# Optimization experiments

Hardware: AMD Instinct MI355X
Metric: run time of the kernel (lower is better)

Reference implementation:

```python
import jax, jax.numpy as jnp
import numpy as np
from jax import lax

NPOINTS = 1024
K = 32
EPS = 1e-5


def fps(xyz, npoints):
    # Furthest point sampling. xyz: (B, N, 3) -> idx (B, npoints) int32.
    B, N, _ = xyz.shape
    def step(carry, _):
        dists, last = carry
        last_xyz = jnp.take_along_axis(xyz, last[:, None, None], axis=1)  # (B,1,3)
        d = jnp.sum((xyz - last_xyz) ** 2, axis=-1)  # (B,N)
        dists = jnp.minimum(dists, d)
        nxt = jnp.argmax(dists, axis=-1).astype(jnp.int32)
        return (dists, nxt), last
    init = (jnp.full((B, N), 1e10, xyz.dtype), jnp.zeros((B,), jnp.int32))
    _, idx = lax.scan(step, init, None, length=npoints)
    return idx.T  # (B, npoints)


def knn_idx(new_xyz, xyz, k):
    # new_xyz (B,S,3), xyz (B,N,3) -> (B,S,k) indices of k nearest neighbors.
    d = (jnp.sum(new_xyz ** 2, -1)[:, :, None]
         - 2.0 * jnp.einsum('bsc,bnc->bsn', new_xyz, xyz)
         + jnp.sum(xyz ** 2, -1)[:, None, :])  # (B,S,N)
    _, idx = lax.top_k(-d, k)
    return idx


def batch_gather(x, idx):
    # x (B, N, C), idx (B, ...) -> (B, ..., C)
    return jax.vmap(lambda a, i: a[i])(x, idx)


def bn(x, g, b, axes):
    # training-mode batchnorm over `axes`, channel on last axis
    m = jnp.mean(x, axes, keepdims=True)
    v = jnp.var(x, axes, keepdims=True)
    return g * (x - m) * lax.rsqrt(v + EPS) + b


def setup_inputs() -> dict:
    key = jax.random.key(0)
    ks = jax.random.split(key, 8)
    B, N, D, Cw, OUT = 16, 4096, 64, 64, 64
    inp = {
        'xyz': jax.random.uniform(ks[0], (B, N, 3), jnp.float32),
        'feature': jax.random.normal(ks[1], (B, D, N), jnp.float32),
        'w0': jax.random.normal(ks[2], (3, Cw), jnp.float32) * 0.3,
        'b0': jnp.zeros((Cw,), jnp.float32),
        'g0': jnp.ones((Cw,), jnp.float32),
        'be0': jnp.zeros((Cw,), jnp.float32),
        'w1': jax.random.normal(ks[3], (Cw, Cw), jnp.float32) * 0.1,
        'b1': jnp.zeros((Cw,), jnp.float32),
        'g1': jnp.ones((Cw,), jnp.float32),
        'be1': jnp.zeros((Cw,), jnp.float32),
        'w2': jax.random.normal(ks[4], (Cw, Cw), jnp.float32) * 0.1,
        'b2': jnp.zeros((Cw,), jnp.float32),
        'g2': jnp.ones((Cw,), jnp.float32),
        'be2': jnp.zeros((Cw,), jnp.float32),
        'wf': jax.random.normal(ks[5], (D * Cw, OUT), jnp.float32) * 0.02,
        'bf': jnp.zeros((OUT,), jnp.float32),
        'gf': jnp.ones((OUT,), jnp.float32),
        'bef': jnp.zeros((OUT,), jnp.float32),
    }
    return inp


def reference(xyz, feature, w0, b0, g0, be0, w1, b1, g1, be1, w2, b2, g2, be2, wf, bf, gf, bef):
    B, N, _ = xyz.shape
    # FPS + gather centroids
    fps_idx = fps(xyz, NPOINTS)                    # (B, S)
    new_xyz = batch_gather(xyz, fps_idx)           # (B, S, 3)
    # kNN grouping
    idx = knn_idx(new_xyz, xyz, K)                 # (B, S, K)
    grouped_xyz = batch_gather(xyz, idx) - new_xyz[:, :, None, :]   # (B,S,K,3)
    feat_nlast = jnp.swapaxes(feature, 1, 2)       # (B, N, D)
    grouped_feature = batch_gather(feat_nlast, idx)  # (B, S, K, D)
    # WeightNet: 1x1 conv MLP 3 -> Cw -> Cw -> Cw with BN+ReLU
    h = grouped_xyz
    for w, b, g, be in ((w0, b0, g0, be0), (w1, b1, g1, be1), (w2, b2, g2, be2)):
        h = jax.nn.relu(bn(h @ w + b, g, be, (0, 1, 2)))  # (B,S,K,Cw)
    weights = h
    # per-centroid matmul: (B,S,D,K) x (B,S,K,Cw) -> (B,S,D,Cw)
    nf = jnp.einsum('bskd,bskw->bsdw', grouped_feature, weights)
    nf = nf.reshape(B, NPOINTS, -1)                # (B, S, D*Cw)
    # final Conv1d(1x1) + BN1d + ReLU
    out = jax.nn.relu(bn(nf @ wf + bf, gf, bef, (0, 1)))  # (B, S, OUT)
    out = jnp.swapaxes(out, 1, 2)                  # (B, OUT, S)
    return (new_xyz, out)
```

## Files before the change

### kernel.cpp

```cpp
#include <hip/hip_runtime.h>

#define NBATCH 16
#define NPTS   4096
#define NSAMP  1024
#define NKNN   32
#define NROWS  (NBATCH*NSAMP*NKNN)
#define BN_EPS 1e-5f
#define H1PAD  66
#define KNN_CAP 512

typedef __attribute__((ext_vector_type(4))) float f32x4;
typedef __attribute__((ext_vector_type(8))) short bf16x8;
union frag_u { unsigned u[4]; bf16x8 h; uint4 u4; };

__device__ __forceinline__ unsigned pack_bf16pair(float a, float b) {
    unsigned ua = __float_as_uint(a); ua += 0x7FFFu + ((ua >> 16) & 1u);
    unsigned ub = __float_as_uint(b); ub += 0x7FFFu + ((ub >> 16) & 1u);
    return (ua >> 16) | (ub & 0xFFFF0000u);
}

__global__ __launch_bounds__(256) void fps_kernel(const float* __restrict__ xyz,
                                                  float* __restrict__ newxyz)
{
    const int b = blockIdx.x;
    const int tid = threadIdx.x;
    const int wv = tid >> 6;
    const float* xb = xyz + (size_t)b * NPTS * 3;
    __shared__ float xs[NPTS];
    __shared__ float ys[NPTS];
    __shared__ float zs[NPTS];
    __shared__ __align__(16) float4 red[2][4];
    __shared__ __align__(16) float nxs[NSAMP*3];
    float px[16], py[16], pz[16], dmin[16];
    {
        float arr[48];
        const float4* s4 = (const float4*)(xb + (size_t)tid * 48);
        #pragma unroll
        for (int i = 0; i < 12; ++i) *(float4*)&arr[i*4] = s4[i];
        #pragma unroll
        for (int j = 0; j < 16; ++j) {
            px[j] = arr[3*j]; py[j] = arr[3*j+1]; pz[j] = arr[3*j+2];
            const int p = tid * 16 + j;
            xs[p] = px[j]; ys[p] = py[j]; zs[p] = pz[j];
            dmin[j] = 1e10f;
        }
    }
    if (tid == 0) { nxs[0] = xb[0]; nxs[1] = xb[1]; nxs[2] = xb[2]; }
    __syncthreads();
    float lx = xs[0], ly = ys[0], lz = zs[0];
    for (int t = 1; t < NSAMP; ++t) {
        float bv = -1.0f;
        #pragma unroll
        for (int j = 0; j < 16; ++j) {
            const float dx = __fsub_rn(px[j], lx);
            const float dy = __fsub_rn(py[j], ly);
            const float dz = __fsub_rn(pz[j], lz);
            const float d = __fadd_rn(__fadd_rn(__fmul_rn(dx,dx), __fmul_rn(dy,dy)), __fmul_rn(dz,dz));
            const float nd = fminf(dmin[j], d);
            dmin[j] = nd;
            bv = fmaxf(bv, nd);
        }
        int lj = 0;
        #pragma unroll
        for (int j = 15; j >= 0; --j) if (dmin[j] == bv) lj = j;
        const int bi_lane = tid * 16 + lj;
        float mv = bv;
        {
            int s_;
            s_ = __builtin_amdgcn_mov_dpp(__float_as_int(mv), 0x111, 0xf, 0xf, true);
            mv = fmaxf(mv, __int_as_float(s_));
            s_ = __builtin_amdgcn_mov_dpp(__float_as_int(mv), 0x112, 0xf, 0xf, true);
            mv = fmaxf(mv, __int_as_float(s_));
            s_ = __builtin_amdgcn_mov_dpp(__float_as_int(mv), 0x114, 0xf, 0xf, true);
            mv = fmaxf(mv, __int_as_float(s_));
            s_ = __builtin_amdgcn_mov_dpp(__float_as_int(mv), 0x118, 0xf, 0xf, true);
            mv = fmaxf(mv, __int_as_float(s_));
            s_ = __builtin_amdgcn_mov_dpp(__float_as_int(mv), 0x142, 0xf, 0xf, true);
            mv = fmaxf(mv, __int_as_float(s_));
            s_ = __builtin_amdgcn_mov_dpp(__float_as_int(mv), 0x143, 0xf, 0xf, true);
            mv = fmaxf(mv, __int_as_float(s_));
        }
        mv = __int_as_float(__builtin_amdgcn_readlane(__float_as_int(mv), 63));
        const unsigned long long mask = __ballot(bv == mv);
        const int winner = __ffsll(mask) - 1;
        const int bi_w = __builtin_amdgcn_readlane(bi_lane, winner);
        const float wx = xs[bi_w], wy = ys[bi_w], wz = zs[bi_w];
        const int par = t & 1;
        if ((tid & 63) == 0) red[par][wv] = make_float4(mv, wx, wy, wz);
        __syncthreads();
        float4 w0 = red[par][0];
        const float4 w1 = red[par][1];
        const float4 w2 = red[par][2];
        const float4 w3 = red[par][3];
        if (w1.x > w0.x) w0 = w1;
        if (w2.x > w0.x) w0 = w2;
        if (w3.x > w0.x) w0 = w3;
        lx = w0.y; ly = w0.z; lz = w0.w;
        if (tid == 0) { nxs[t*3] = lx; nxs[t*3+1] = ly; nxs[t*3+2] = lz; }
    }
    __syncthreads();
    {
        float4* d4 = (float4*)(newxyz + (size_t)b * NSAMP * 3);
        const float4* s4 = (const float4*)nxs;
        #pragma unroll
        for (int i = tid; i < NSAMP*3/4; i += 256) d4[i] = s4[i];
    }
}

__device__ __forceinline__ void bin_select(int* hist, int* ctrl, int* wsum,
                                           int tid, int shift)
{
    const int lane = tid & 63, wv = tid >> 6;
    const int cnt = hist[tid];
    const int r = ctrl[1];
    int incl = cnt;
    #pragma unroll
    for (int d = 1; d < 64; d <<= 1) {
        const int v = __shfl_up(incl, d);
        if (lane >= d) incl += v;
    }
    if (lane == 63) wsum[wv] = incl;
    __syncthreads();
    int base = 0;
    if (wv > 0) base += wsum[0];
    if (wv > 1) base += wsum[1];
    if (wv > 2) base += wsum[2];
    incl += base;
    const int excl = incl - cnt;
    if (excl < r && r <= incl) {
        ctrl[0] |= tid << shift;
        ctrl[1] = r - excl;
        ctrl[2] = cnt;
    }
}

__global__ __launch_bounds__(256) void knn_kernel(const float* __restrict__ xyz,
                                                  const float* __restrict__ newxyz,
                                                  int* __restrict__ idx_out)
{
    const int bs = blockIdx.x;
    const int b = bs >> 10;
    const int tid = threadIdx.x;
    __shared__ unsigned keys[NPTS];
    __shared__ int hist[256];
    __shared__ float qsh[3];
    __shared__ int ctrl[8];
    __shared__ int wsum[4];
    __shared__ int cl[KNN_CAP];
    __shared__ int lt[32];
    __shared__ int ties[128];
    if (tid < 3) qsh[tid] = newxyz[bs*3 + tid];
    if (tid == 0) { ctrl[0] = 0; ctrl[1] = NKNN; }
    hist[tid] = 0;
    __syncthreads();
    const float q0 = qsh[0], q1 = qsh[1], q2 = qsh[2];
    const float qq = __fadd_rn(__fadd_rn(__fmul_rn(q0,q0), __fmul_rn(q1,q1)), __fmul_rn(q2,q2));
    const float* xb = xyz + (size_t)b * NPTS * 3;
    for (int n = tid; n < NPTS; n += 256) {
        const float x0 = xb[n*3+0], x1 = xb[n*3+1], x2 = xb[n*3+2];
        const float xx = __fadd_rn(__fadd_rn(__fmul_rn(x0,x0), __fmul_rn(x1,x1)), __fmul_rn(x2,x2));
        float dt = __fmul_rn(q0, x0);
        dt = __fmaf_rn(q1, x1, dt);
        dt = __fmaf_rn(q2, x2, dt);
        const float dd = __fadd_rn(__fsub_rn(qq, __fmul_rn(2.0f, dt)), xx);
        unsigned ub = __float_as_uint(dd);
        ub = (ub & 0x80000000u) ? ~ub : (ub | 0x80000000u);
        keys[n] = ub;
        atomicAdd(&hist[ub >> 24], 1);
    }
    __syncthreads();
    bin_select(hist, ctrl, wsum, tid, 24);
    __syncthreads();
    const unsigned pf3 = (unsigned)ctrl[0];
    const int bin3 = (int)(pf3 >> 24);
    const int m = ctrl[2];
    const bool compact = (m <= KNN_CAP);
    if (tid == 0) { ctrl[3] = 0; ctrl[4] = 0; ctrl[5] = 0; ctrl[6] = 0; }
    __syncthreads();
    if (compact) {
        for (int n = tid; n < NPTS; n += 256) {
            const int tb = (int)(keys[n] >> 24);
            if (tb == bin3)      { const int pos = atomicAdd(&ctrl[3], 1); cl[pos] = n; }
            else if (tb < bin3)  { const int pos = atomicAdd(&ctrl[4], 1); lt[pos] = n; }
        }
    }
    __syncthreads();
    for (int p = 2; p >= 0; --p) {
        hist[tid] = 0;
        __syncthreads();
        const unsigned pre = (unsigned)ctrl[0];
        const int shift = p * 8;
        const unsigned himask = 0xFFFFFFFFu << ((p + 1) * 8);
        if (compact) {
            const int eqn = ctrl[3];
            for (int i = tid; i < eqn; i += 256) {
                const unsigned k = keys[cl[i]];
                if ((k & himask) == pre) atomicAdd(&hist[(k >> shift) & 255], 1);
            }
        } else {
            for (int n = tid; n < NPTS; n += 256) {
                const unsigned k = keys[n];
                if ((k & himask) == pre) atomicAdd(&hist[(k >> shift) & 255], 1);
            }
        }
        __syncthreads();
        bin_select(hist, ctrl, wsum, tid, shift);
        __syncthreads();
    }
    const unsigned T = (unsigned)ctrl[0];
    int* out = idx_out + (size_t)bs * NKNN;
    if (compact) {
        const int ltn = ctrl[4];
        if (tid == 0) ctrl[5] = ltn;
        __syncthreads();
        if (tid < ltn) out[tid] = lt[tid];
        const int eqn = ctrl[3];
        for (int i = tid; i < eqn; i += 256) {
            const int n = cl[i];
            const unsigned k = keys[n];
            if (k < T) {
                const int pos = atomicAdd(&ctrl[5], 1);
                if (pos < NKNN) out[pos] = n;
            } else if (k == T) {
                const int pos = atomicAdd(&ctrl[6], 1);
                if (pos < 128) ties[pos] = n;
            }
        }
    } else {
        for (int n = tid; n < NPTS; n += 256) {
            const unsigned k = keys[n];
            if (k < T) {
                const int pos = atomicAdd(&ctrl[5], 1);
                if (pos < NKNN) out[pos] = n;
            } else if (k == T) {
                const int pos = atomicAdd(&ctrl[6], 1);
                if (pos < 128) ties[pos] = n;
            }
        }
    }
    __syncthreads();
    if (tid == 0) {
        const int nless = ctrl[5] < NKNN ? ctrl[5] : NKNN;
        const int need = NKNN - nless;
        const int ntie = ctrl[6] < 128 ? ctrl[6] : 128;
        int last = -1;
        for (int j = 0; j < need; ++j) {
            int best = 0x7fffffff;
            for (int i = 0; i < ntie; ++i) {
                const int v = ties[i];
                if (v > last && v < best) best = v;
            }
            out[nless + j] = (best == 0x7fffffff) ? 0 : best;
            last = best;
        }
    }
}

__global__ void zero_all_kernel(double* st, float* g1, float* g2)
{
    const int i = blockIdx.x * 256 + threadIdx.x;
    if (i < 512) st[i] = 0.0;
    if (i < 4096) { g1[i] = 0.f; g2[i] = 0.f; }
}

__global__ __launch_bounds__(256) void gxmoments_kernel(
    const float* __restrict__ xyz, const float* __restrict__ newxyz,
    const int* __restrict__ idxws, double* __restrict__ stats)
{
    const int tid = threadIdx.x;
    double m[9];
    #pragma unroll
    for (int i = 0; i < 9; ++i) m[i] = 0.0;
    for (int row = blockIdx.x * 256 + tid; row < NROWS; row += gridDim.x * 256) {
        const int bs = row >> 5;
        const int bb = row >> 15;
        const int id = idxws[row];
        const float* xp = xyz + ((size_t)bb * NPTS + id) * 3;
        const float* qp = newxyz + bs * 3;
        const double dx = (double)(xp[0] - qp[0]);
        const double dy = (double)(xp[1] - qp[1]);
        const double dz = (double)(xp[2] - qp[2]);
        m[0] += dx; m[1] += dy; m[2] += dz;
        m[3] += dx*dx; m[4] += dx*dy; m[5] += dx*dz;
        m[6] += dy*dy; m[7] += dy*dz; m[8] += dz*dz;
    }
    #pragma unroll
    for (int i = 0; i < 9; ++i) {
        #pragma unroll
        for (int s = 1; s < 64; s <<= 1) m[i] += __shfl_xor(m[i], s);
    }
    __shared__ double part[4][9];
    if ((tid & 63) == 0) {
        #pragma unroll
        for (int i = 0; i < 9; ++i) part[tid >> 6][i] = m[i];
    }
    __syncthreads();
    if (tid < 9) atomicAdd(&stats[tid], part[0][tid] + part[1][tid] + part[2][tid] + part[3][tid]);
}

__global__ void bn0_moments_finalize_kernel(const double* __restrict__ st,
    const float* __restrict__ w0, const float* __restrict__ b0,
    const float* __restrict__ g0, const float* __restrict__ be0,
    float* __restrict__ outp)
{
    const int c = threadIdx.x;
    const double N = (double)NROWS;
    const double w0c = w0[c], w1c = w0[64 + c], w2c = w0[128 + c];
    const double b = b0[c];
    const double dotS = st[0]*w0c + st[1]*w1c + st[2]*w2c;
    const double qf = w0c*w0c*st[3] + w1c*w1c*st[6] + w2c*w2c*st[8]
                    + 2.0*(w0c*w1c*st[4] + w0c*w2c*st[5] + w1c*w2c*st[7]);
    const double mean = dotS / N + b;
    const double ex2 = (qf + 2.0*b*dotS) / N + b*b;
    const double var = ex2 - mean*mean;
    const float scale = g0[c] * rsqrtf((float)var + BN_EPS);
    outp[c] = scale;
    outp[64 + c] = be0[c] - (float)mean * scale;
}

__global__ void wfpack_kernel(const float* __restrict__ wf, unsigned* __restrict__ wfb)
{
    const int blk = blockIdx.x;
    const int kt = blk >> 2, ot = blk & 3;
    const int l = threadIdx.x;
    const int o = ot*16 + (l & 15);
    const int kb = kt*32 + (l >> 4)*8;
    unsigned out[4];
    #pragma unroll
    for (int r = 0; r < 4; ++r) {
        const float a = wf[(size_t)(kb + 2*r) * 64 + o];
        const float b = wf[(size_t)(kb + 2*r + 1) * 64 + o];
        out[r] = pack_bf16pair(a, b);
    }
    *(uint4*)&wfb[((size_t)blk * 64 + l) * 4] = *(const uint4*)out;
}

__global__ __launch_bounds__(256) void gram1_kernel(
    const float* __restrict__ xyz, const float* __restrict__ newxyz,
    const int* __restrict__ idxws,
    const float* __restrict__ w0, const float* __restrict__ b0,
    const float* __restrict__ bnp, float* __restrict__ G1,
    double* __restrict__ Sh1)
{
    __shared__ float gxs[32][3];
    __shared__ float h1s[32][H1PAD];
    __shared__ float rsum[256];
    const int tid = threadIdx.x;
    const int c = tid & 63;
    const int rq = tid >> 6;
    const int lg = c >> 4, lm = c & 15;
    const float w0c0 = w0[c], w0c1 = w0[64+c], w0c2 = w0[128+c];
    const float b0c = b0[c], sc0 = bnp[c], sh0 = bnp[64+c];
    f32x4 Ga[4] = {{0,0,0,0},{0,0,0,0},{0,0,0,0},{0,0,0,0}};
    float sumh = 0.f;
    for (int chunk = blockIdx.x; chunk < NROWS/32; chunk += gridDim.x) {
        if (tid < 96) {
            const int slot = tid / 3, cc = tid % 3;
            const int row = chunk*32 + slot;
            const int bs = row >> 5, bb = row >> 15;
            gxs[slot][cc] = xyz[((size_t)bb * NPTS + idxws[row]) * 3 + cc] - newxyz[bs*3 + cc];
        }
        __syncthreads();
        #pragma unroll
        for (int i = 0; i < 8; ++i) {
            const int r = rq*8 + i;
            const float t0 = gxs[r][0]*w0c0 + gxs[r][1]*w0c1 + gxs[r][2]*w0c2 + b0c;
            const float h = fmaxf(sc0*t0 + sh0, 0.f);
            h1s[r][c] = h;
            sumh += h;
        }
        __syncthreads();
        frag_u fr[4];
        #pragma unroll
        for (int ct = 0; ct < 4; ++ct)
            #pragma unroll
            for (int r = 0; r < 4; ++r)
                fr[ct].u[r] = pack_bf16pair(h1s[lg*8 + 2*r][ct*16 + lm],
                                            h1s[lg*8 + 2*r + 1][ct*16 + lm]);
        #pragma unroll
        for (int ct = 0; ct < 4; ++ct)
            Ga[ct] = __builtin_amdgcn_mfma_f32_16x16x32_bf16(fr[rq].h, fr[ct].h, Ga[ct], 0, 0, 0);
        __syncthreads();
    }
    #pragma unroll
    for (int ct = 0; ct < 4; ++ct)
        #pragma unroll
        for (int r = 0; r < 4; ++r)
            atomicAdd(&G1[(rq*16 + lg*4 + r)*64 + ct*16 + lm], Ga[ct][r]);
    rsum[tid] = sumh;
    __syncthreads();
    if (tid < 64) atomicAdd(&Sh1[c], (double)(rsum[c] + rsum[64+c] + rsum[128+c] + rsum[192+c]));
}

__global__ __launch_bounds__(256) void gram2_kernel(
    const float* __restrict__ xyz, const float* __restrict__ newxyz,
    const int* __restrict__ idxws,
    const float* __restrict__ w0, const float* __restrict__ b0,
    const float* __restrict__ b1, const unsigned* __restrict__ w1b,
    const float* __restrict__ bnp, float* __restrict__ G2,
    double* __restrict__ Sh2)
{
    __shared__ float gxs[32][3];
    __shared__ float h1s[32][H1PAD];
    __shared__ float h2s[32][H1PAD];
    __shared__ float rsum[256];
    const int tid = threadIdx.x;
    const int c = tid & 63;
    const int rq = tid >> 6;
    const int lg = c >> 4, lm = c & 15;
    const int c2 = rq*16 + lm;
    const float w0c0 = w0[c], w0c1 = w0[64+c], w0c2 = w0[128+c];
    const float b0c = b0[c], sc0 = bnp[c], sh0 = bnp[64+c];
    const float b1c2 = b1[c2], sc1 = bnp[128+c2], sh1 = bnp[192+c2];
    frag_u Bw1[2];
    Bw1[0].u4 = *(const uint4*)&w1b[((0*4 + rq)*64 + c)*4];
    Bw1[1].u4 = *(const uint4*)&w1b[((1*4 + rq)*64 + c)*4];
    f32x4 Ga[4] = {{0,0,0,0},{0,0,0,0},{0,0,0,0},{0,0,0,0}};
    float sumh = 0.f;
    for (int chunk = blockIdx.x; chunk < NROWS/32; chunk += gridDim.x) {
        if (tid < 96) {
            const int slot = tid / 3, cc = tid % 3;
            const int row = chunk*32 + slot;
            const int bs = row >> 5, bb = row >> 15;
            gxs[slot][cc] = xyz[((size_t)bb * NPTS + idxws[row]) * 3 + cc] - newxyz[bs*3 + cc];
        }
        __syncthreads();
        #pragma unroll
        for (int i = 0; i < 8; ++i) {
            const int r = rq*8 + i;
            const float t0 = gxs[r][0]*w0c0 + gxs[r][1]*w0c1 + gxs[r][2]*w0c2 + b0c;
            h1s[r][c] = fmaxf(sc0*t0 + sh0, 0.f);
        }
        __syncthreads();
        #pragma unroll
        for (int mt = 0; mt < 2; ++mt) {
            f32x4 acc = {0,0,0,0};
            #pragma unroll
            for (int kt = 0; kt < 2; ++kt) {
                frag_u a;
                #pragma unroll
                for (int r = 0; r < 4; ++r) {
                    const float2 f = *(const float2*)&h1s[mt*16 + lm][kt*32 + lg*8 + 2*r];
                    a.u[r] = pack_bf16pair(f.x, f.y);
                }
                acc = __builtin_amdgcn_mfma_f32_16x16x32_bf16(a.h, Bw1[kt].h, acc, 0, 0, 0);
            }
            #pragma unroll
            for (int r = 0; r < 4; ++r)
                h2s[mt*16 + lg*4 + r][c2] = fmaxf(sc1*(acc[r] + b1c2) + sh1, 0.f);
        }
        __syncthreads();
        #pragma unroll
        for (int i = 0; i < 8; ++i) sumh += h2s[rq*8 + i][c];
        frag_u fr[4];
        #pragma unroll
        for (int ct = 0; ct < 4; ++ct)
            #pragma unroll
            for (int r = 0; r < 4; ++r)
                fr[ct].u[r] = pack_bf16pair(h2s[lg*8 + 2*r][ct*16 + lm],
                                            h2s[lg*8 + 2*r + 1][ct*16 + lm]);
        #pragma unroll
        for (int ct = 0; ct < 4; ++ct)
            Ga[ct] = __builtin_amdgcn_mfma_f32_16x16x32_bf16(fr[rq].h, fr[ct].h, Ga[ct], 0, 0, 0);
        __syncthreads();
    }
    #pragma unroll
    for (int ct = 0; ct < 4; ++ct)
        #pragma unroll
        for (int r = 0; r < 4; ++r)
            atomicAdd(&G2[(rq*16 + lg*4 + r)*64 + ct*16 + lm], Ga[ct][r]);
    rsum[tid] = sumh;
    __syncthreads();
    if (tid < 64) atomicAdd(&Sh2[c], (double)(rsum[c] + rsum[64+c] + rsum[128+c] + rsum[192+c]));
}

__global__ __launch_bounds__(256) void bn_gram_finalize_kernel(
    const double* __restrict__ Sh, const float* __restrict__ G,
    const float* __restrict__ w, const float* __restrict__ bias,
    const float* __restrict__ g, const float* __restrict__ be,
    float* __restrict__ outp)
{
    __shared__ float wls[64][65];
    __shared__ double shl[64];
    __shared__ double rd[256], rqd[256];
    const int tid = threadIdx.x;
    const int c = tid & 63;
    const int rqi = tid >> 6;
    for (int i = tid; i < 4096; i += 256) wls[i >> 6][i & 63] = w[i];
    if (tid < 64) shl[tid] = Sh[tid];
    __syncthreads();
    double dot = 0.0, quad = 0.0;
    for (int j = rqi*16; j < rqi*16 + 16; ++j) {
        const double wjc = (double)wls[j][c];
        dot += wjc * shl[j];
        double inner = 0.0;
        for (int k = 0; k < 64; ++k) inner += (double)G[j*64 + k] * (double)wls[k][c];
        quad += wjc * inner;
    }
    rd[tid] = dot; rqd[tid] = quad;
    __syncthreads();
    if (tid < 64) {
        const double d = rd[c] + rd[64+c] + rd[128+c] + rd[192+c];
        const double q = rqd[c] + rqd[64+c] + rqd[128+c] + rqd[192+c];
        const double N = (double)NROWS;
        const double bc = (double)bias[c];
        const double mean = d / N + bc;
        const double ex2 = (q + 2.0*bc*d) / N + bc*bc;
        const double var = ex2 - mean*mean;
        const float scale = g[c] * rsqrtf((float)var + BN_EPS);
        outp[c] = scale;
        outp[64 + c] = be[c] - (float)mean * scale;
    }
}

__global__ void bn_finalize_kernel(const double* __restrict__ st,
                                   const float* __restrict__ g,
                                   const float* __restrict__ be,
                                   float* __restrict__ outp, float n)
{
    const int c = threadIdx.x;
    const double m = st[c] / (double)n;
    const double var = st[64 + c] / (double)n - m * m;
    const float scale = g[c] * rsqrtf((float)var + BN_EPS);
    outp[c] = scale;
    outp[64 + c] = be[c] - (float)m * scale;
}

__global__ __launch_bounds__(256) void final_conv_kernel(
    const float* __restrict__ xyz, const float* __restrict__ newxyz,
    const int* __restrict__ idxws, const float* __restrict__ feat,
    const float* __restrict__ w0, const float* __restrict__ b0,
    const float* __restrict__ b1, const float* __restrict__ b2,
    const float* __restrict__ bnp, const unsigned* __restrict__ wfb,
    const unsigned* __restrict__ w1b, const unsigned* __restrict__ w2b,
    const float* __restrict__ bf, float* __restrict__ y)
{
    __shared__ unsigned wtp[8][16][64];
    __shared__ __align__(16) float scratch[2*64*H1PAD];
    __shared__ float gxs[64][3];
    __shared__ int   idxs[8][32];
    __shared__ float qs[8][3];
    float* h1s = scratch;
    float* h2s = scratch + 64*H1PAD;
    unsigned* yaf = (unsigned*)scratch;
    const int tid = threadIdx.x;
    const int c = tid & 63;
    const int rq = tid >> 6;
    const int lg = c >> 4, lm = c & 15;
    const int c2 = rq*16 + lm;
    const int bs0 = blockIdx.x * 8;
    const int b = bs0 >> 10;
    idxs[tid >> 5][tid & 31] = idxws[(size_t)bs0 * NKNN + tid];
    if (tid < 24)  qs[tid / 3][tid % 3] = newxyz[(bs0 + tid/3)*3 + (tid % 3)];
    const float w0c0 = w0[c], w0c1 = w0[64+c], w0c2 = w0[128+c];
    const float b0c = b0[c], sc0 = bnp[c], sh0 = bnp[64+c];
    const float b1c2 = b1[c2], sc1 = bnp[128+c2], sh1 = bnp[192+c2];
    const float b2c2 = b2[c2], sc2 = bnp[256+c2], sh2 = bnp[320+c2];
    frag_u Bw1[2], Bw2[2];
    #pragma unroll
    for (int kt = 0; kt < 2; ++kt) {
        Bw1[kt].u4 = *(const uint4*)&w1b[((kt*4 + rq)*64 + c)*4];
        Bw2[kt].u4 = *(const uint4*)&w2b[((kt*4 + rq)*64 + c)*4];
    }
    __syncthreads();
    for (int chunk = 0; chunk < 4; ++chunk) {
        if (tid < 192) {
            const int slot = tid / 3, cc = tid % 3;
            const int grow = chunk*64 + slot;
            const int e = grow >> 5, k = grow & 31;
            gxs[slot][cc] = xyz[((size_t)b * NPTS + idxs[e][k]) * 3 + cc] - qs[e][cc];
        }
        __syncthreads();
        #pragma unroll
        for (int i = 0; i < 16; ++i) {
            const int r = rq*16 + i;
            const float t0 = gxs[r][0]*w0c0 + gxs[r][1]*w0c1 + gxs[r][2]*w0c2 + b0c;
            h1s[r*H1PAD + c] = fmaxf(sc0*t0 + sh0, 0.f);
        }
        __syncthreads();
        #pragma unroll
        for (int mt = 0; mt < 4; ++mt) {
            f32x4 acc = {0,0,0,0};
            #pragma unroll
            for (int kt = 0; kt < 2; ++kt) {
                frag_u a;
                #pragma unroll
                for (int r = 0; r < 4; ++r) {
                    const float2 f = *(const float2*)&h1s[(mt*16 + lm)*H1PAD + kt*32 + lg*8 + 2*r];
                    a.u[r] = pack_bf16pair(f.x, f.y);
                }
                acc = __builtin_amdgcn_mfma_f32_16x16x32_bf16(a.h, Bw1[kt].h, acc, 0, 0, 0);
            }
            #pragma unroll
            for (int r = 0; r < 4; ++r)
                h2s[(mt*16 + lg*4 + r)*H1PAD + c2] = fmaxf(sc1*(acc[r] + b1c2) + sh1, 0.f);
        }
        __syncthreads();
        #pragma unroll
        for (int mt = 0; mt < 4; ++mt) {
            f32x4 acc = {0,0,0,0};
            #pragma unroll
            for (int kt = 0; kt < 2; ++kt) {
                frag_u a;
                #pragma unroll
                for (int r = 0; r < 4; ++r) {
                    const float2 f = *(const float2*)&h2s[(mt*16 + lm)*H1PAD + kt*32 + lg*8 + 2*r];
                    a.u[r] = pack_bf16pair(f.x, f.y);
                }
                acc = __builtin_amdgcn_mfma_f32_16x16x32_bf16(a.h, Bw2[kt].h, acc, 0, 0, 0);
            }
            float wt[4];
            #pragma unroll
            for (int r = 0; r < 4; ++r)
                wt[r] = fmaxf(sc2*(acc[r] + b2c2) + sh2, 0.f);
            const int grow0 = chunk*64 + mt*16 + lg*4;
            const int e = grow0 >> 5, kl = grow0 & 31;
            wtp[e][kl >> 1][c2]       = pack_bf16pair(wt[0], wt[1]);
            wtp[e][(kl >> 1) + 1][c2] = pack_bf16pair(wt[2], wt[3]);
        }
        __syncthreads();
    }
    const int lane = c;
    const int wid = rq;
    frag_u afr[2][4];
    #pragma unroll
    for (int es = 0; es < 2; ++es)
        #pragma unroll
        for (int w4 = 0; w4 < 4; ++w4)
            #pragma unroll
            for (int r = 0; r < 4; ++r)
                afr[es][w4].u[r] = wtp[wid*2 + es][lg*4 + r][w4*16 + lm];
    f32x4 yacc = {0.f, 0.f, 0.f, 0.f};
    for (int dhalf = 0; dhalf < 2; ++dhalf) {
        #pragma unroll
        for (int es = 0; es < 2; ++es) {
            const int e = wid*2 + es;
            #pragma unroll
            for (int dt = 0; dt < 2; ++dt) {
                const int d = dhalf*32 + dt*16 + lm;
                const float* fb = feat + (size_t)(b*64 + d) * NPTS;
                frag_u B;
                #pragma unroll
                for (int r = 0; r < 4; ++r) {
                    const int k0 = lg*8 + 2*r;
                    B.u[r] = pack_bf16pair(fb[idxs[e][k0]], fb[idxs[e][k0+1]]);
                }
                #pragma unroll
                for (int w4 = 0; w4 < 4; ++w4) {
                    f32x4 dnf = {0.f, 0.f, 0.f, 0.f};
                    dnf = __builtin_amdgcn_mfma_f32_16x16x32_bf16(afr[es][w4].h, B.h, dnf, 0, 0, 0);
                    const unsigned p0 = pack_bf16pair(dnf[0], dnf[1]);
                    const unsigned p1 = pack_bf16pair(dnf[2], dnf[3]);
                    const int dloc = dt*16 + lm;
                    const int kp0 = dloc*32 + w4*8 + lg*2;
                    const int sw = kp0 ^ ((lm & 3) << 3) ^ ((e & 7) << 2);
                    *(uint2*)&yaf[e*1024 + sw] = make_uint2(p0, p1);
                }
            }
        }
        __syncthreads();
        for (int kt = 0; kt < 64; ++kt) {
            frag_u A, Bf;
            const int kpb = (kt*16 + lg*4) ^ (((kt >> 1) & 3) << 3) ^ ((lm & 7) << 2);
            A.u4 = *(const uint4*)&yaf[(lm & 7)*1024 + kpb];
            Bf.u4 = *(const uint4*)&wfb[(((size_t)(dhalf*64 + kt)*4 + wid)*64 + lane)*4];
            yacc = __builtin_amdgcn_mfma_f32_16x16x32_bf16(A.h, Bf.h, yacc, 0, 0, 0);
        }
        __syncthreads();
    }
    if (lg < 2) {
        const float bfo = bf[wid*16 + lm];
        #pragma unroll
        for (int r = 0; r < 4; ++r)
            y[(size_t)(bs0 + lg*4 + r) * 64 + wid*16 + lm] = yacc[r] + bfo;
    }
}

__global__ __launch_bounds__(256) void ystats_kernel(const float* __restrict__ y,
                                                     double* __restrict__ st)
{
    const int tid = threadIdx.x;
    const int c = tid & 63;
    double s = 0.0, s2 = 0.0;
    for (int i = blockIdx.x * 256 + tid; i < NBATCH*NSAMP*64; i += gridDim.x * 256) {
        const float v = y[i];
        s += v; s2 += (double)v * (double)v;
    }
    __shared__ double rs[256], rs2[256];
    rs[tid] = s; rs2[tid] = s2;
    __syncthreads();
    if (tid < 64) {
        const double a  = rs[c]  + rs[64+c]  + rs[128+c]  + rs[192+c];
        const double a2 = rs2[c] + rs2[64+c] + rs2[128+c] + rs2[192+c];
        atomicAdd(&st[c], a);
        atomicAdd(&st[64 + c], a2);
    }
}

__global__ void writeout_kernel(const float* __restrict__ y,
                                const float* __restrict__ bnp3,
                                float* __restrict__ outp)
{
    const int i = blockIdx.x * 256 + threadIdx.x;
    if (i >= NBATCH * 64 * NSAMP) return;
    const int s = i & 1023;
    const int o = (i >> 10) & 63;
    const int bb = i >> 16;
    const float v = y[((size_t)(bb << 10) + s) * 64 + o];
    outp[i] = fmaxf(bnp3[o] * v + bnp3[64 + o], 0.f);
}

extern "C" void kernel_launch(void* const* d_in, const int* in_sizes, int n_in,
                              void* d_out, int out_size, void* d_ws, size_t ws_size,
                              hipStream_t stream)
{
    (void)in_sizes; (void)n_in; (void)out_size; (void)ws_size;
    const float* xyz  = (const float*)d_in[0];
    const float* feat = (const float*)d_in[1];
    const float* w0   = (const float*)d_in[2];
    const float* b0   = (const float*)d_in[3];
    const float* g0   = (const float*)d_in[4];
    const float* be0  = (const float*)d_in[5];
    const float* w1   = (const float*)d_in[6];
    const float* b1   = (const float*)d_in[7];
    const float* g1   = (const float*)d_in[8];
    const float* be1  = (const float*)d_in[9];
    const float* w2   = (const float*)d_in[10];
    const float* b2   = (const float*)d_in[11];
    const float* g2   = (const float*)d_in[12];
    const float* be2  = (const float*)d_in[13];
    const float* wf   = (const float*)d_in[14];
    const float* bf   = (const float*)d_in[15];
    const float* gf   = (const float*)d_in[16];
    const float* bef  = (const float*)d_in[17];

    float* out = (float*)d_out;
    float* newxyz = out;
    float* outmain = out + NBATCH * NSAMP * 3;

    char* ws = (char*)d_ws;
    int*      idxws = (int*)ws;
    float*    ybuf  = (float*)(ws + 2097152);
    double*   stats = (double*)(ws + 6291456);
    float*    bnp   = (float*)(ws + 6295552);
    unsigned* wfb   = (unsigned*)(ws + 6297600);
    unsigned* w1b   = (unsigned*)(ws + 6821888);
    unsigned* w2b   = (unsigned*)(ws + 6830080);
    float*    G1    = (float*)(ws + 6838272);
    float*    G2    = (float*)(ws + 6854656);

    zero_all_kernel<<<16, 256, 0, stream>>>(stats, G1, G2);
    wfpack_kernel<<<512, 64, 0, stream>>>(wf, wfb);
    wfpack_kernel<<<8, 64, 0, stream>>>(w1, w1b);
    wfpack_kernel<<<8, 64, 0, stream>>>(w2, w2b);
    fps_kernel<<<NBATCH, 256, 0, stream>>>(xyz, newxyz);
    knn_kernel<<<NBATCH * NSAMP, 256, 0, stream>>>(xyz, newxyz, idxws);

    gxmoments_kernel<<<512, 256, 0, stream>>>(xyz, newxyz, idxws, stats);
    bn0_moments_finalize_kernel<<<1, 64, 0, stream>>>(stats, w0, b0, g0, be0, bnp);
    gram1_kernel<<<256, 256, 0, stream>>>(xyz, newxyz, idxws, w0, b0, bnp, G1, stats + 128);
    bn_gram_finalize_kernel<<<1, 256, 0, stream>>>(stats + 128, G1, w1, b1, g1, be1, bnp + 128);
    gram2_kernel<<<256, 256, 0, stream>>>(xyz, newxyz, idxws, w0, b0, b1, w1b, bnp, G2, stats + 192);
    bn_gram_finalize_kernel<<<1, 256, 0, stream>>>(stats + 192, G2, w2, b2, g2, be2, bnp + 256);

    final_conv_kernel<<<NBATCH * NSAMP / 8, 256, 0, stream>>>(
        xyz, newxyz, idxws, feat, w0, b0, b1, b2, bnp, wfb, w1b, w2b, bf, ybuf);

    ystats_kernel<<<256, 256, 0, stream>>>(ybuf, stats + 384);
    bn_finalize_kernel<<<1, 64, 0, stream>>>(stats + 384, gf, bef, bnp + 384, (float)(NBATCH * NSAMP));
    writeout_kernel<<<4096, 256, 0, stream>>>(ybuf, bnp + 384, outmain);
}
```

Baseline: 1.371 ms.

## Merge weight packing launches, float moments, preload grouped xyz, dual MFMA accumulators

Several unrelated tweaks land together. The three weight-packing launches become one kernel. gxmoments accumulates in float per thread, converts to double only for the reduction, and uses twice as many blocks. final_conv gathers all 256 grouped-xyz rows once before the chunk loop instead of once per chunk with a barrier each time. The final MFMA reduction loop is split across two independent accumulators to shorten the dependency chain. These cut launch overhead, FP64 work and barriers, at the cost of more shared memory and slightly lower-precision moment accumulation.

```diff
diff --git a/kernel.cpp b/kernel.cpp
--- a/kernel.cpp
+++ b/kernel.cpp
@@ -268,31 +268,33 @@
     const int* __restrict__ idxws, double* __restrict__ stats)
 {
     const int tid = threadIdx.x;
-    double m[9];
+    float m[9];
     #pragma unroll
-    for (int i = 0; i < 9; ++i) m[i] = 0.0;
+    for (int i = 0; i < 9; ++i) m[i] = 0.f;
     for (int row = blockIdx.x * 256 + tid; row < NROWS; row += gridDim.x * 256) {
         const int bs = row >> 5;
         const int bb = row >> 15;
         const int id = idxws[row];
         const float* xp = xyz + ((size_t)bb * NPTS + id) * 3;
         const float* qp = newxyz + bs * 3;
-        const double dx = (double)(xp[0] - qp[0]);
-        const double dy = (double)(xp[1] - qp[1]);
-        const double dz = (double)(xp[2] - qp[2]);
+        const float dx = xp[0] - qp[0];
+        const float dy = xp[1] - qp[1];
+        const float dz = xp[2] - qp[2];
         m[0] += dx; m[1] += dy; m[2] += dz;
         m[3] += dx*dx; m[4] += dx*dy; m[5] += dx*dz;
         m[6] += dy*dy; m[7] += dy*dz; m[8] += dz*dz;
     }
+    double d[9];
     #pragma unroll
     for (int i = 0; i < 9; ++i) {
-        #pragma unroll
-        for (int s = 1; s < 64; s <<= 1) m[i] += __shfl_xor(m[i], s);
+        d[i] = (double)m[i];
+        #pragma unroll
+        for (int s = 1; s < 64; s <<= 1) d[i] += __shfl_xor(d[i], s);
     }
     __shared__ double part[4][9];
     if ((tid & 63) == 0) {
         #pragma unroll
-        for (int i = 0; i < 9; ++i) part[tid >> 6][i] = m[i];
+        for (int i = 0; i < 9; ++i) part[tid >> 6][i] = d[i];
     }
     __syncthreads();
     if (tid < 9) atomicAdd(&stats[tid], part[0][tid] + part[1][tid] + part[2][tid] + part[3][tid]);
@@ -318,9 +320,18 @@
     outp[64 + c] = be0[c] - (float)mean * scale;
 }
 
-__global__ void wfpack_kernel(const float* __restrict__ wf, unsigned* __restrict__ wfb)
-{
-    const int blk = blockIdx.x;
+__global__ void wfpack_all_kernel(const float* __restrict__ wf,
+                                  const float* __restrict__ w1,
+                                  const float* __restrict__ w2,
+                                  unsigned* __restrict__ wfb,
+                                  unsigned* __restrict__ w1b,
+                                  unsigned* __restrict__ w2b)
+{
+    int blk = blockIdx.x;
+    const float* src; unsigned* dst;
+    if (blk < 512)      { src = wf; dst = wfb; }
+    else if (blk < 520) { src = w1; dst = w1b; blk -= 512; }
+    else                { src = w2; dst = w2b; blk -= 520; }
     const int kt = blk >> 2, ot = blk & 3;
     const int l = threadIdx.x;
     const int o = ot*16 + (l & 15);
@@ -328,11 +339,11 @@
     unsigned out[4];
     #pragma unroll
     for (int r = 0; r < 4; ++r) {
-        const float a = wf[(size_t)(kb + 2*r) * 64 + o];
-        const float b = wf[(size_t)(kb + 2*r + 1) * 64 + o];
+        const float a = src[(size_t)(kb + 2*r) * 64 + o];
+        const float b = src[(size_t)(kb + 2*r + 1) * 64 + o];
         out[r] = pack_bf16pair(a, b);
     }
-    *(uint4*)&wfb[((size_t)blk * 64 + l) * 4] = *(const uint4*)out;
+    *(uint4*)&dst[((size_t)blk * 64 + l) * 4] = *(const uint4*)out;
 }
 
 __global__ __launch_bounds__(256) void gram1_kernel(
@@ -537,7 +548,7 @@
 {
     __shared__ unsigned wtp[8][16][64];
     __shared__ __align__(16) float scratch[2*64*H1PAD];
-    __shared__ float gxs[64][3];
+    __shared__ float gxs[256][3];
     __shared__ int   idxs[8][32];
     __shared__ float qs[8][3];
     float* h1s = scratch;
@@ -563,18 +574,18 @@
         Bw2[kt].u4 = *(const uint4*)&w2b[((kt*4 + rq)*64 + c)*4];
     }
     __syncthreads();
+    for (int i = tid; i < 768; i += 256) {
+        const int row = i / 3, cc = i - row * 3;
+        const int e = row >> 5, k = row & 31;
+        gxs[row][cc] = xyz[((size_t)b * NPTS + idxs[e][k]) * 3 + cc] - qs[e][cc];
+    }
+    __syncthreads();
     for (int chunk = 0; chunk < 4; ++chunk) {
-        if (tid < 192) {
-            const int slot = tid / 3, cc = tid % 3;
-            const int grow = chunk*64 + slot;
-            const int e = grow >> 5, k = grow & 31;
-            gxs[slot][cc] = xyz[((size_t)b * NPTS + idxs[e][k]) * 3 + cc] - qs[e][cc];
-        }
-        __syncthreads();
         #pragma unroll
         for (int i = 0; i < 16; ++i) {
             const int r = rq*16 + i;
-            const float t0 = gxs[r][0]*w0c0 + gxs[r][1]*w0c1 + gxs[r][2]*w0c2 + b0c;
+            const int gr = chunk*64 + r;
+            const float t0 = gxs[gr][0]*w0c0 + gxs[gr][1]*w0c1 + gxs[gr][2]*w0c2 + b0c;
             h1s[r*H1PAD + c] = fmaxf(sc0*t0 + sh0, 0.f);
         }
         __syncthreads();
@@ -630,7 +641,8 @@
             #pragma unroll
             for (int r = 0; r < 4; ++r)
                 afr[es][w4].u[r] = wtp[wid*2 + es][lg*4 + r][w4*16 + lm];
-    f32x4 yacc = {0.f, 0.f, 0.f, 0.f};
+    f32x4 yaccA = {0.f, 0.f, 0.f, 0.f};
+    f32x4 yaccB = {0.f, 0.f, 0.f, 0.f};
     for (int dhalf = 0; dhalf < 2; ++dhalf) {
         #pragma unroll
         for (int es = 0; es < 2; ++es) {
@@ -659,12 +671,16 @@
             }
         }
         __syncthreads();
-        for (int kt = 0; kt < 64; ++kt) {
-            frag_u A, Bf;
-            const int kpb = (kt*16 + lg*4) ^ (((kt >> 1) & 3) << 3) ^ ((lm & 7) << 2);
-            A.u4 = *(const uint4*)&yaf[(lm & 7)*1024 + kpb];
-            Bf.u4 = *(const uint4*)&wfb[(((size_t)(dhalf*64 + kt)*4 + wid)*64 + lane)*4];
-            yacc = __builtin_amdgcn_mfma_f32_16x16x32_bf16(A.h, Bf.h, yacc, 0, 0, 0);
+        for (int kt = 0; kt < 64; kt += 2) {
+            frag_u A0, B0, A1, B1;
+            const int kpb0 = (kt*16 + lg*4) ^ (((kt >> 1) & 3) << 3) ^ ((lm & 7) << 2);
+            const int kpb1 = ((kt+1)*16 + lg*4) ^ ((((kt+1) >> 1) & 3) << 3) ^ ((lm & 7) << 2);
+            A0.u4 = *(const uint4*)&yaf[(lm & 7)*1024 + kpb0];
+            A1.u4 = *(const uint4*)&yaf[(lm & 7)*1024 + kpb1];
+            B0.u4 = *(const uint4*)&wfb[(((size_t)(dhalf*64 + kt)*4 + wid)*64 + lane)*4];
+            B1.u4 = *(const uint4*)&wfb[(((size_t)(dhalf*64 + kt + 1)*4 + wid)*64 + lane)*4];
+            yaccA = __builtin_amdgcn_mfma_f32_16x16x32_bf16(A0.h, B0.h, yaccA, 0, 0, 0);
+            yaccB = __builtin_amdgcn_mfma_f32_16x16x32_bf16(A1.h, B1.h, yaccB, 0, 0, 0);
         }
         __syncthreads();
     }
@@ -672,7 +688,7 @@
         const float bfo = bf[wid*16 + lm];
         #pragma unroll
         for (int r = 0; r < 4; ++r)
-            y[(size_t)(bs0 + lg*4 + r) * 64 + wid*16 + lm] = yacc[r] + bfo;
+            y[(size_t)(bs0 + lg*4 + r) * 64 + wid*16 + lm] = (yaccA[r] + yaccB[r]) + bfo;
     }
 }
 
@@ -750,13 +766,11 @@
     float*    G2    = (float*)(ws + 6854656);
 
     zero_all_kernel<<<16, 256, 0, stream>>>(stats, G1, G2);
-    wfpack_kernel<<<512, 64, 0, stream>>>(wf, wfb);
-    wfpack_kernel<<<8, 64, 0, stream>>>(w1, w1b);
-    wfpack_kernel<<<8, 64, 0, stream>>>(w2, w2b);
+    wfpack_all_kernel<<<528, 64, 0, stream>>>(wf, w1, w2, wfb, w1b, w2b);
     fps_kernel<<<NBATCH, 256, 0, stream>>>(xyz, newxyz);
     knn_kernel<<<NBATCH * NSAMP, 256, 0, stream>>>(xyz, newxyz, idxws);
 
-    gxmoments_kernel<<<512, 256, 0, stream>>>(xyz, newxyz, idxws, stats);
+    gxmoments_kernel<<<1024, 256, 0, stream>>>(xyz, newxyz, idxws, stats);
     bn0_moments_finalize_kernel<<<1, 64, 0, stream>>>(stats, w0, b0, g0, be0, bnp);
     gram1_kernel<<<256, 256, 0, stream>>>(xyz, newxyz, idxws, w0, b0, bnp, G1, stats + 128);
     bn_gram_finalize_kernel<<<1, 256, 0, stream>>>(stats + 128, G1, w1, b1, g1, be1, bnp + 128);
```

Result: no change. 1.396 ms (+1.8%).
